# Kernel optimization log

Measured on AMD Instinct MI355X. Metric: run time of the kernel, lower is better.

The kernel has to match this reference:

```python
import jax, jax.numpy as jnp
import numpy as np

KERNEL = 3
STRIDE = 1
PAD = 1


def setup_inputs() -> dict:
    key = jax.random.key(0)
    k1, k2 = jax.random.split(key)
    x = jax.random.normal(k1, (16, 32, 512, 512), dtype=jnp.float32)
    # original init: torch.rand(O, I, k, k) / (k*k)
    kernels = jax.random.uniform(k2, (32, 32, KERNEL, KERNEL), dtype=jnp.float32) / (KERNEL * KERNEL)
    return {"x": x, "kernels": kernels}


def reference(x, kernels):
    # Equivalent math to the unfold+einsum im2col conv2d: pad, extract kxk
    # windows with stride, contract over (in_channels, kh, kw).
    # Expressed as a direct convolution (cross-correlation), which is the
    # same computation without materializing the 6D window tensor.
    out = jax.lax.conv_general_dilated(
        x, kernels,
        window_strides=(STRIDE, STRIDE),
        padding=((PAD, PAD), (PAD, PAD)),
        dimension_numbers=("NCHW", "OIHW", "NCHW"),
    )
    return out  # [B, out_channels, H_out, W_out]
```

## Files before the change

### kernel.cpp

```cpp
#include <hip/hip_runtime.h>
#include <hip/hip_bf16.h>

typedef __attribute__((ext_vector_type(8))) short bf16x8;
typedef __attribute__((ext_vector_type(4))) float f32x4;
typedef __attribute__((ext_vector_type(4))) unsigned int u32x4;

#define HW (512 * 512)
#define TW 64
#define SLOTS 6
#define PXG (SLOTS * 66)
#define TILE_B (4 * PXG * 16)
#define STAGE_HALF 20480
#define SREAL 18432
#define DUMMY (TILE_B + 2 * STAGE_HALF)
#define NITER 32

#define SCHED() __builtin_amdgcn_sched_barrier(0)

__device__ __forceinline__ unsigned short f2bf(float f) {
    unsigned u = __builtin_bit_cast(unsigned, f);
    u += 0x7FFFu + ((u >> 16) & 1u);
    return (unsigned short)(u >> 16);
}

__device__ __forceinline__ void gll16(const float* g, char* l) {
    __builtin_amdgcn_global_load_lds(
        (const __attribute__((address_space(1))) void*)g,
        (__attribute__((address_space(3))) void*)l, 16, 0, 0);
}

__device__ __forceinline__ void issue_stage(const float* __restrict__ xb, int row0,
                                            int w0, char* smem, int half, int wvu) {
    const int lane = (int)threadIdx.x & 63;
    char* base = smem + TILE_B + half * STAGE_HALF;
    #pragma unroll
    for (int i = 0; i < 5; ++i) {
        int ob = (wvu * 5 + i) * 1024;
        int o  = ob + lane * 16;
        int o2 = o < (SREAL - 1) ? o : (SREAL - 1);
        int ch = o2 / 576;
        int rem = o2 - ch * 576;
        int hh = rem / 288;
        int wl = (rem - hh * 288) >> 2;
        int row = row0 + hh; row = row < 511 ? row : 511;
        int cb = w0 - 4 + wl;
        cb = cb < 0 ? 0 : (cb > 508 ? 508 : cb);
        gll16(xb + (size_t)ch * HW + row * 512 + cb, base + ob);
    }
}

template<bool TRANS, bool GLL, bool BAR>
__device__ __forceinline__ void body(char* smem, const float* __restrict__ xb,
                                     float* __restrict__ ob, bf16x8 (&wf)[9][2],
                                     int srb, int half, int rowbase, int w0,
                                     int wv, int wvu, int col16, int g4) {
    if (GLL) issue_stage(xb, rowbase + 5, w0, smem, half ^ 1, wvu);

    if (TRANS) {
        const char* sb = smem + TILE_B + half * STAGE_HALF;
        const int rowA = rowbase + 3;
        #pragma unroll
        for (int k = 0; k < 3; ++k) {
            if (k == 2 && threadIdx.x >= 32) continue;
            int u = (k < 2) ? (int)threadIdx.x + k * 256 : 512 + (int)threadIdx.x;
            int g = u / 136, r = u - g * 136, sl = r / 68, ww = r - sl * 68;
            float v[8];
            int ba = g * 8 * 576 + sl * 288 + (ww + 3) * 4;
            #pragma unroll
            for (int j = 0; j < 8; ++j) v[j] = *(const float*)(sb + ba + j * 576);
            bool ok = (ww < 66) & ((unsigned)(w0 + ww - 1) < 512u) & (rowA + sl < 512);
            #pragma unroll
            for (int j = 0; j < 8; ++j) v[j] = ok ? v[j] : 0.f;
            unsigned q0 = (unsigned)f2bf(v[0]) | ((unsigned)f2bf(v[1]) << 16);
            unsigned q1 = (unsigned)f2bf(v[2]) | ((unsigned)f2bf(v[3]) << 16);
            unsigned q2 = (unsigned)f2bf(v[4]) | ((unsigned)f2bf(v[5]) << 16);
            unsigned q3 = (unsigned)f2bf(v[6]) | ((unsigned)f2bf(v[7]) << 16);
            int slot = srb + 4 + sl; if (slot >= SLOTS) slot -= SLOTS;
            int byte = (ww < 66) ? (g * PXG + slot * 66 + ww) * 16
                                 : (DUMMY + ((int)threadIdx.x & 63) * 16);
            u32x4 q = { q0, q1, q2, q3 };
            *(u32x4*)(smem + byte) = q;
        }
    }

    f32x4 acc[2][2];
    {
        f32x4 z = {0.f, 0.f, 0.f, 0.f};
        acc[0][0] = z; acc[0][1] = z; acc[1][0] = z; acc[1][1] = z;
    }
    int rs[3];
    #pragma unroll
    for (int dh = 0; dh < 3; ++dh) {
        int s = srb + (wv & 1) + dh; if (s >= SLOTS) s -= SLOTS;
        rs[dh] = s * 66;
    }
    const int wcb = (wv >> 1) * 32;
    const char* xg = smem + g4 * (PXG * 16);
    #pragma unroll
    for (int dh = 0; dh < 3; ++dh) {
        #pragma unroll
        for (int dw = 0; dw < 3; ++dw) {
            const int tap = dh * 3 + dw;
            #pragma unroll
            for (int m = 0; m < 2; ++m) {
                bf16x8 a = *(const bf16x8*)(xg + (rs[dh] + wcb + m * 16 + col16 + dw) * 16);
                acc[m][0] = __builtin_amdgcn_mfma_f32_16x16x32_bf16(a, wf[tap][0], acc[m][0], 0, 0, 0);
                acc[m][1] = __builtin_amdgcn_mfma_f32_16x16x32_bf16(a, wf[tap][1], acc[m][1], 0, 0, 0);
            }
        }
    }
    {
        float* orow = ob + (size_t)(rowbase + (wv & 1)) * 512 + w0 + wcb;
        #pragma unroll
        for (int m = 0; m < 2; ++m)
            #pragma unroll
            for (int n = 0; n < 2; ++n)
                *(f32x4*)(orow + (size_t)(n * 16 + col16) * HW + m * 16 + g4 * 4) = acc[m][n];
    }

    if (BAR) {
        asm volatile("s_waitcnt vmcnt(4)" ::: "memory");
        SCHED();
        asm volatile("s_waitcnt lgkmcnt(0)" ::: "memory");
        SCHED();
        __builtin_amdgcn_s_barrier();
        SCHED();
    }
}

__global__ __launch_bounds__(256, 2)
void conv3x3_mfma(const float* __restrict__ x,
                  const float* __restrict__ wk,
                  float* __restrict__ out) {
    __shared__ __align__(16) char smem[DUMMY + 1024];

    const int tid   = (int)threadIdx.x;
    const int lane  = tid & 63;
    const int wv    = tid >> 6;
    const int wvu   = __builtin_amdgcn_readfirstlane(wv);
    const int col16 = lane & 15;
    const int g4    = lane >> 4;

    const int w0    = blockIdx.x * TW;
    const int hbase = blockIdx.y * 64;
    const int b     = blockIdx.z;

    const float* xb = x + (size_t)b * 32 * HW;
    float* ob = out + (size_t)b * 32 * HW;

    {
        float* ws = (float*)(smem + TILE_B);
        for (int i = tid; i < 9216; i += 256) {
            int oc = i / 288;
            ws[oc * 289 + (i - oc * 288)] = wk[i];
        }
    }
    float svp[5][8];
    #pragma unroll
    for (int k = 0; k < 5; ++k) {
        if (k == 4 && tid >= 32) continue;
        int u = (k < 4) ? tid + k * 256 : 1024 + tid;
        int g = u / 264, p = u - g * 264, hh = p / 66, ww = p - hh * 66;
        int row = hbase + hh - 1, cl = w0 + ww - 1;
        bool ok = ((unsigned)row < 512u) & ((unsigned)cl < 512u);
        int rowc = row < 0 ? 0 : (row > 511 ? 511 : row);
        int clc  = cl  < 0 ? 0 : (cl  > 511 ? 511 : cl);
        const float* src = xb + (size_t)(g * 8) * HW + rowc * 512 + clc;
        #pragma unroll
        for (int j = 0; j < 8; ++j) { float v = src[(size_t)j * HW]; svp[k][j] = ok ? v : 0.f; }
    }
    __syncthreads();

    bf16x8 wf[9][2];
    {
        const float* ws = (const float*)(smem + TILE_B);
        #pragma unroll
        for (int tap = 0; tap < 9; ++tap) {
            #pragma unroll
            for (int n = 0; n < 2; ++n) {
                bf16x8 f;
                #pragma unroll
                for (int j = 0; j < 8; ++j)
                    f[j] = (short)f2bf(ws[(n * 16 + col16) * 289 + (g4 * 8 + j) * 9 + tap]);
                wf[tap][n] = f;
            }
        }
    }
    __syncthreads();

    #pragma unroll
    for (int k = 0; k < 5; ++k) {
        if (k == 4 && tid >= 32) continue;
        int u = (k < 4) ? tid + k * 256 : 1024 + tid;
        int g = u / 264, p = u - g * 264;
        unsigned q0 = (unsigned)f2bf(svp[k][0]) | ((unsigned)f2bf(svp[k][1]) << 16);
        unsigned q1 = (unsigned)f2bf(svp[k][2]) | ((unsigned)f2bf(svp[k][3]) << 16);
        unsigned q2 = (unsigned)f2bf(svp[k][4]) | ((unsigned)f2bf(svp[k][5]) << 16);
        unsigned q3 = (unsigned)f2bf(svp[k][6]) | ((unsigned)f2bf(svp[k][7]) << 16);
        u32x4 q = { q0, q1, q2, q3 };
        *(u32x4*)(smem + (g * PXG + p) * 16) = q;
    }
    issue_stage(xb, hbase + 3, w0, smem, 0, wvu);
    __syncthreads();

    int srb = 0;
    #pragma unroll 1
    for (int t = 0; t < 30; ++t) {
        body<1, 1, 1>(smem, xb, ob, wf, srb, t & 1, hbase + 2 * t, w0, wv, wvu, col16, g4);
        srb += 2; if (srb >= SLOTS) srb -= SLOTS;
    }
    body<1, 0, 1>(smem, xb, ob, wf, srb, 0, hbase + 60, w0, wv, wvu, col16, g4);
    srb += 2; if (srb >= SLOTS) srb -= SLOTS;
    body<0, 0, 0>(smem, xb, ob, wf, srb, 1, hbase + 62, w0, wv, wvu, col16, g4);
}

extern "C" void kernel_launch(void* const* d_in, const int* in_sizes, int n_in,
                              void* d_out, int out_size, void* d_ws, size_t ws_size,
                              hipStream_t stream) {
    const float* x  = (const float*)d_in[0];
    const float* wk = (const float*)d_in[1];
    float* out = (float*)d_out;
    dim3 grid(512 / TW, 512 / 64, 16);
    conv3x3_mfma<<<grid, 256, 0, stream>>>(x, wk, out);
}
```

Baseline: 273.5 us.

## Replace LDS staging with register-prefetched rows in a triple-buffered pipeline

Removes the global_load_lds fp32 staging area and the per-iteration LDS transpose pass. Upcoming input rows are now loaded straight into registers (three rotating register sets, two stages ahead) and converted to bf16 only when written into the slot ring, with explicit vmcnt waits set to the pipeline depth. Weight fragments are also read directly from global memory instead of through an LDS copy, which drops two block barriers at startup. The change cuts LDS footprint and LDS traffic per stage, in exchange for many more VGPRs for in-flight loads, which may cost occupancy or cause spills. Each load now carries only 4 bytes instead of 16.

```diff
diff --git a/kernel.cpp b/kernel.cpp
--- a/kernel.cpp
+++ b/kernel.cpp
@@ -10,10 +10,7 @@
 #define SLOTS 6
 #define PXG (SLOTS * 66)
 #define TILE_B (4 * PXG * 16)
-#define STAGE_HALF 20480
-#define SREAL 18432
-#define DUMMY (TILE_B + 2 * STAGE_HALF)
-#define NITER 32
+#define DUMMY TILE_B
 
 #define SCHED() __builtin_amdgcn_sched_barrier(0)
 
@@ -23,65 +20,57 @@
     return (unsigned short)(u >> 16);
 }
 
-__device__ __forceinline__ void gll16(const float* g, char* l) {
-    __builtin_amdgcn_global_load_lds(
-        (const __attribute__((address_space(1))) void*)g,
-        (__attribute__((address_space(3))) void*)l, 16, 0, 0);
-}
-
-__device__ __forceinline__ void issue_stage(const float* __restrict__ xb, int row0,
-                                            int w0, char* smem, int half, int wvu) {
-    const int lane = (int)threadIdx.x & 63;
-    char* base = smem + TILE_B + half * STAGE_HALF;
-    #pragma unroll
-    for (int i = 0; i < 5; ++i) {
-        int ob = (wvu * 5 + i) * 1024;
-        int o  = ob + lane * 16;
-        int o2 = o < (SREAL - 1) ? o : (SREAL - 1);
-        int ch = o2 / 576;
-        int rem = o2 - ch * 576;
-        int hh = rem / 288;
-        int wl = (rem - hh * 288) >> 2;
-        int row = row0 + hh; row = row < 511 ? row : 511;
-        int cb = w0 - 4 + wl;
-        cb = cb < 0 ? 0 : (cb > 508 ? 508 : cb);
-        gll16(xb + (size_t)ch * HW + row * 512 + cb, base + ob);
-    }
-}
-
-template<bool TRANS, bool GLL, bool BAR>
+__device__ __forceinline__ void issueB(const float* __restrict__ xb, int row0, int w0,
+                                       float (&sv)[3][8]) {
+    #pragma unroll
+    for (int k = 0; k < 3; ++k) {
+        int u = (int)threadIdx.x + k * 256;
+        int g = u / 192, r = u - g * 192, hh = r / 96, ww = r - hh * 96;
+        int wwc = ww < 66 ? ww : 65;
+        int row = row0 + hh;
+        int cl  = w0 + wwc - 1;
+        bool ok = (ww < 66) & (row < 512) & ((unsigned)cl < 512u);
+        int rowc = row < 512 ? row : 511;
+        int clc  = cl < 0 ? 0 : (cl > 511 ? 511 : cl);
+        const float* src = xb + (size_t)(g * 8) * HW + rowc * 512 + clc;
+        #pragma unroll
+        for (int j = 0; j < 8; ++j) { float v = src[(size_t)j * HW]; sv[k][j] = ok ? v : 0.f; }
+    }
+}
+
+__device__ __forceinline__ void writeB(char* smem, int wsb, float (&sv)[3][8]) {
+    #pragma unroll
+    for (int k = 0; k < 3; ++k) {
+        int u = (int)threadIdx.x + k * 256;
+        int g = u / 192, r = u - g * 192, hh = r / 96, ww = r - hh * 96;
+        int slot = wsb + hh; if (slot >= SLOTS) slot -= SLOTS;
+        int byte = (ww < 66) ? (g * PXG + slot * 66 + ww) * 16
+                             : (DUMMY + ((int)threadIdx.x & 63) * 16);
+        unsigned q0 = (unsigned)f2bf(sv[k][0]) | ((unsigned)f2bf(sv[k][1]) << 16);
+        unsigned q1 = (unsigned)f2bf(sv[k][2]) | ((unsigned)f2bf(sv[k][3]) << 16);
+        unsigned q2 = (unsigned)f2bf(sv[k][4]) | ((unsigned)f2bf(sv[k][5]) << 16);
+        unsigned q3 = (unsigned)f2bf(sv[k][6]) | ((unsigned)f2bf(sv[k][7]) << 16);
+        u32x4 q = { q0, q1, q2, q3 };
+        *(u32x4*)(smem + byte) = q;
+    }
+}
+
+template<int W, bool WR, bool ISS, bool BAR>
 __device__ __forceinline__ void body(char* smem, const float* __restrict__ xb,
                                      float* __restrict__ ob, bf16x8 (&wf)[9][2],
-                                     int srb, int half, int rowbase, int w0,
-                                     int wv, int wvu, int col16, int g4) {
-    if (GLL) issue_stage(xb, rowbase + 5, w0, smem, half ^ 1, wvu);
-
-    if (TRANS) {
-        const char* sb = smem + TILE_B + half * STAGE_HALF;
-        const int rowA = rowbase + 3;
-        #pragma unroll
-        for (int k = 0; k < 3; ++k) {
-            if (k == 2 && threadIdx.x >= 32) continue;
-            int u = (k < 2) ? (int)threadIdx.x + k * 256 : 512 + (int)threadIdx.x;
-            int g = u / 136, r = u - g * 136, sl = r / 68, ww = r - sl * 68;
-            float v[8];
-            int ba = g * 8 * 576 + sl * 288 + (ww + 3) * 4;
-            #pragma unroll
-            for (int j = 0; j < 8; ++j) v[j] = *(const float*)(sb + ba + j * 576);
-            bool ok = (ww < 66) & ((unsigned)(w0 + ww - 1) < 512u) & (rowA + sl < 512);
-            #pragma unroll
-            for (int j = 0; j < 8; ++j) v[j] = ok ? v[j] : 0.f;
-            unsigned q0 = (unsigned)f2bf(v[0]) | ((unsigned)f2bf(v[1]) << 16);
-            unsigned q1 = (unsigned)f2bf(v[2]) | ((unsigned)f2bf(v[3]) << 16);
-            unsigned q2 = (unsigned)f2bf(v[4]) | ((unsigned)f2bf(v[5]) << 16);
-            unsigned q3 = (unsigned)f2bf(v[6]) | ((unsigned)f2bf(v[7]) << 16);
-            int slot = srb + 4 + sl; if (slot >= SLOTS) slot -= SLOTS;
-            int byte = (ww < 66) ? (g * PXG + slot * 66 + ww) * 16
-                                 : (DUMMY + ((int)threadIdx.x & 63) * 16);
-            u32x4 q = { q0, q1, q2, q3 };
-            *(u32x4*)(smem + byte) = q;
-        }
-    }
+                                     float (&cur)[3][8], float (&nxt)[3][8],
+                                     int srb, int rowbase, int w0,
+                                     int wv, int col16, int g4) {
+    if constexpr (W == 24) { asm volatile("s_waitcnt vmcnt(24)" ::: "memory"); SCHED(); }
+    else if constexpr (W == 28) { asm volatile("s_waitcnt vmcnt(28)" ::: "memory"); SCHED(); }
+    else if constexpr (W == 32) { asm volatile("s_waitcnt vmcnt(32)" ::: "memory"); SCHED(); }
+    else if constexpr (W == 8)  { asm volatile("s_waitcnt vmcnt(8)"  ::: "memory"); SCHED(); }
+
+    if (WR) {
+        int wsb = srb + 4; if (wsb >= SLOTS) wsb -= SLOTS;
+        writeB(smem, wsb, cur);
+    }
+    if (ISS) issueB(xb, rowbase + 7, w0, nxt);
 
     f32x4 acc[2][2];
     {
@@ -117,10 +106,7 @@
             for (int n = 0; n < 2; ++n)
                 *(f32x4*)(orow + (size_t)(n * 16 + col16) * HW + m * 16 + g4 * 4) = acc[m][n];
     }
-
     if (BAR) {
-        asm volatile("s_waitcnt vmcnt(4)" ::: "memory");
-        SCHED();
         asm volatile("s_waitcnt lgkmcnt(0)" ::: "memory");
         SCHED();
         __builtin_amdgcn_s_barrier();
@@ -132,12 +118,11 @@
 void conv3x3_mfma(const float* __restrict__ x,
                   const float* __restrict__ wk,
                   float* __restrict__ out) {
-    __shared__ __align__(16) char smem[DUMMY + 1024];
+    __shared__ __align__(16) char smem[TILE_B + 1024];
 
     const int tid   = (int)threadIdx.x;
     const int lane  = tid & 63;
     const int wv    = tid >> 6;
-    const int wvu   = __builtin_amdgcn_readfirstlane(wv);
     const int col16 = lane & 15;
     const int g4    = lane >> 4;
 
@@ -148,20 +133,13 @@
     const float* xb = x + (size_t)b * 32 * HW;
     float* ob = out + (size_t)b * 32 * HW;
 
-    {
-        float* ws = (float*)(smem + TILE_B);
-        for (int i = tid; i < 9216; i += 256) {
-            int oc = i / 288;
-            ws[oc * 289 + (i - oc * 288)] = wk[i];
-        }
-    }
     float svp[5][8];
     #pragma unroll
     for (int k = 0; k < 5; ++k) {
         if (k == 4 && tid >= 32) continue;
         int u = (k < 4) ? tid + k * 256 : 1024 + tid;
-        int g = u / 264, p = u - g * 264, hh = p / 66, ww = p - hh * 66;
-        int row = hbase + hh - 1, cl = w0 + ww - 1;
+        int g = u / 264, p = u - g * 264;
+        int row = hbase + p / 66 - 1, cl = w0 + p % 66 - 1;
         bool ok = ((unsigned)row < 512u) & ((unsigned)cl < 512u);
         int rowc = row < 0 ? 0 : (row > 511 ? 511 : row);
         int clc  = cl  < 0 ? 0 : (cl  > 511 ? 511 : cl);
@@ -169,24 +147,19 @@
         #pragma unroll
         for (int j = 0; j < 8; ++j) { float v = src[(size_t)j * HW]; svp[k][j] = ok ? v : 0.f; }
     }
-    __syncthreads();
 
     bf16x8 wf[9][2];
-    {
-        const float* ws = (const float*)(smem + TILE_B);
-        #pragma unroll
-        for (int tap = 0; tap < 9; ++tap) {
+    #pragma unroll
+    for (int tap = 0; tap < 9; ++tap) {
+        #pragma unroll
+        for (int n = 0; n < 2; ++n) {
+            bf16x8 f;
             #pragma unroll
-            for (int n = 0; n < 2; ++n) {
-                bf16x8 f;
-                #pragma unroll
-                for (int j = 0; j < 8; ++j)
-                    f[j] = (short)f2bf(ws[(n * 16 + col16) * 289 + (g4 * 8 + j) * 9 + tap]);
-                wf[tap][n] = f;
-            }
+            for (int j = 0; j < 8; ++j)
+                f[j] = (short)f2bf(wk[(n * 16 + col16) * 288 + (g4 * 8 + j) * 9 + tap]);
+            wf[tap][n] = f;
         }
     }
-    __syncthreads();
 
     #pragma unroll
     for (int k = 0; k < 5; ++k) {
@@ -200,18 +173,35 @@
         u32x4 q = { q0, q1, q2, q3 };
         *(u32x4*)(smem + (g * PXG + p) * 16) = q;
     }
-    issue_stage(xb, hbase + 3, w0, smem, 0, wvu);
-    __syncthreads();
-
-    int srb = 0;
+
+    float svA[3][8], svB[3][8], svC[3][8];
+    SCHED();
+    issueB(xb, hbase + 3, w0, svA);
+    issueB(xb, hbase + 5, w0, svB);
+    SCHED();
+    asm volatile("s_waitcnt lgkmcnt(0)" ::: "memory");
+    SCHED();
+    __builtin_amdgcn_s_barrier();
+    SCHED();
+
+    body<24, 1, 1, 1>(smem, xb, ob, wf, svA, svC, 0, hbase,     w0, wv, col16, g4);
+    body<28, 1, 1, 1>(smem, xb, ob, wf, svB, svA, 2, hbase + 2, w0, wv, col16, g4);
+    int srb = 4;
     #pragma unroll 1
-    for (int t = 0; t < 30; ++t) {
-        body<1, 1, 1>(smem, xb, ob, wf, srb, t & 1, hbase + 2 * t, w0, wv, wvu, col16, g4);
+    for (int tq = 0; tq < 9; ++tq) {
+        int t0 = 2 + 3 * tq;
+        body<32, 1, 1, 1>(smem, xb, ob, wf, svC, svB, srb, hbase + 2 * t0,       w0, wv, col16, g4);
         srb += 2; if (srb >= SLOTS) srb -= SLOTS;
-    }
-    body<1, 0, 1>(smem, xb, ob, wf, srb, 0, hbase + 60, w0, wv, wvu, col16, g4);
+        body<32, 1, 1, 1>(smem, xb, ob, wf, svA, svC, srb, hbase + 2 * (t0 + 1), w0, wv, col16, g4);
+        srb += 2; if (srb >= SLOTS) srb -= SLOTS;
+        body<32, 1, 1, 1>(smem, xb, ob, wf, svB, svA, srb, hbase + 2 * (t0 + 2), w0, wv, col16, g4);
+        srb += 2; if (srb >= SLOTS) srb -= SLOTS;
+    }
+    body<32, 1, 0, 1>(smem, xb, ob, wf, svC, svB, srb, hbase + 58, w0, wv, col16, g4);
     srb += 2; if (srb >= SLOTS) srb -= SLOTS;
-    body<0, 0, 0>(smem, xb, ob, wf, srb, 1, hbase + 62, w0, wv, wvu, col16, g4);
+    body<8, 1, 0, 1>(smem, xb, ob, wf, svA, svB, srb, hbase + 60, w0, wv, col16, g4);
+    srb += 2; if (srb >= SLOTS) srb -= SLOTS;
+    body<-1, 0, 0, 0>(smem, xb, ob, wf, svB, svC, srb, hbase + 62, w0, wv, col16, g4);
 }
 
 extern "C" void kernel_launch(void* const* d_in, const int* in_sizes, int n_in,
```

Result: slower. 311.2 us (+13.8%).
